# Optimization experiments

Hardware: AMD Instinct MI355X
Metric: run time of the kernel (lower is better)

The kernel has to match this reference:

```python
import jax, jax.numpy as jnp
import numpy as np

B, T, D, H = 4, 2048, 512, 8
DK = D // H

def setup_inputs() -> dict:
    key = jax.random.key(0)
    ks = jax.random.split(key, 5)
    s = 1.0 / np.sqrt(D)
    return {
        "x": jax.random.normal(ks[0], (B, T, D), dtype=jnp.float32),
        "Wq": jax.random.normal(ks[1], (D, D), dtype=jnp.float32) * s,
        "bq": jnp.zeros((D,), dtype=jnp.float32),
        "Wk": jax.random.normal(ks[2], (D, D), dtype=jnp.float32) * s,
        "bk": jnp.zeros((D,), dtype=jnp.float32),
        "Wv": jax.random.normal(ks[3], (D, D), dtype=jnp.float32) * s,
        "bv": jnp.zeros((D,), dtype=jnp.float32),
        "Wo": jax.random.normal(ks[4], (D, D), dtype=jnp.float32) * s,
        "bo": jnp.zeros((D,), dtype=jnp.float32),
    }

def reference(x, Wq, bq, Wk, bk, Wv, bv, Wo, bo):
    # Linear projections (torch Linear: x @ W.T + b); split into heads.
    q = (x @ Wq.T + bq).reshape(B, T, H, DK)  # [B,T,H,dk]
    k = (x @ Wk.T + bk).reshape(B, T, H, DK)
    v = (x @ Wv.T + bv).reshape(B, T, H, DK)
    scale = 1.0 / np.sqrt(DK)
    # scores: [B,H,T,T]
    scores = jnp.einsum("bqhd,bkhd->bhqk", q, k) * scale
    attn = jax.nn.softmax(scores, axis=-1)
    ctx = jnp.einsum("bhqk,bkhd->bqhd", attn, v).reshape(B, T, D)
    return ctx @ Wo.T + bo
```

## Files before the change

kernel.cpp:

```cpp
#include <hip/hip_runtime.h>
#include <stdint.h>

#define NB 4
#define NT 2048
#define ND 512
#define NH 8
#define NDK 64
#define NM (NB*NT)

typedef __attribute__((ext_vector_type(8))) short short8;
typedef __attribute__((ext_vector_type(4))) float f32x4;

__device__ __forceinline__ unsigned short f2b(float f) {
    union { float f; uint32_t u; } v; v.f = f;
    return (unsigned short)((v.u + 0x7FFFu + ((v.u >> 16) & 1u)) >> 16);
}

__device__ __forceinline__ void load_lds16(const void* g, void* l) {
    void* gn = const_cast<void*>(g);
    __builtin_amdgcn_global_load_lds((__attribute__((address_space(1))) void*)gn,
                                     (__attribute__((address_space(3))) void*)l,
                                     16, 0, 0);
}

__global__ void convert_all(const float* __restrict__ x,  const float* __restrict__ wq,
                            const float* __restrict__ wk, const float* __restrict__ wv,
                            const float* __restrict__ wo, unsigned short* __restrict__ dst) {
    size_t i = ((size_t)blockIdx.x * 256 + threadIdx.x) * 4;
    const float* src; size_t off;
    if (i < 4194304) { src = x; off = i; }
    else {
        size_t j = i - 4194304;
        src = (j < 262144) ? wq : (j < 524288) ? wk : (j < 786432) ? wv : wo;
        off = j & 262143;
    }
    f32x4 v = *(const f32x4*)(src + off);
    ushort4 r;
    r.x = f2b(v[0]); r.y = f2b(v[1]); r.z = f2b(v[2]); r.w = f2b(v[3]);
    *(ushort4*)(dst + i) = r;
}

__global__ __launch_bounds__(256, 3) void proj_gemm(
        const unsigned short* __restrict__ X,
        const unsigned short* __restrict__ Wbase,
        const float* __restrict__ bias0, const float* __restrict__ bias1,
        const float* __restrict__ bias2,
        unsigned short* __restrict__ Obase, unsigned short* __restrict__ VTb,
        float scale0) {
    const int z = blockIdx.z;
    const float* bias = (z == 0) ? bias0 : (z == 1 ? bias1 : bias2);
    const float scale = (z == 0) ? scale0 : 1.0f;

    int rowBase, colBase;
    const unsigned short *Ap, *Bp;
    if (z == 2) {
        rowBase = blockIdx.x * 128;  colBase = blockIdx.y * 128;
        Ap = Wbase + 2 * (ND * ND);  Bp = X;
    } else {
        rowBase = blockIdx.y * 128;  colBase = blockIdx.x * 128;
        Ap = X;                      Bp = Wbase + (size_t)z * (ND * ND);
    }

    __shared__ alignas(16) unsigned short ldsA[128 * 64];
    __shared__ alignas(16) unsigned short ldsW[128 * 64];

    const int tid = threadIdx.x;
    const int lane = tid & 63, wave = tid >> 6;
    const int quad = lane >> 4, l15 = lane & 15;
    const int wm = wave >> 1, wn = wave & 1;

    const int rS = tid >> 3;
    const int gc = (tid & 7) ^ (rS & 7);
    const unsigned short* gA = Ap + (size_t)(rowBase + rS) * ND + gc * 8;
    const unsigned short* gW = Bp + (size_t)(colBase + rS) * ND + gc * 8;
    const int ldst = wave * 512;

    const int swz = l15 & 7;

    f32x4 acc[4][4];
#pragma unroll
    for (int i = 0; i < 4; i++)
#pragma unroll
        for (int j = 0; j < 4; j++) acc[i][j] = (f32x4)0.0f;

    for (int kt = 0; kt < ND / 64; ++kt) {
        __syncthreads();
#pragma unroll
        for (int c = 0; c < 4; ++c) {
            load_lds16(gA + (size_t)c * 32 * ND, ldsA + c * 2048 + ldst);
            load_lds16(gW + (size_t)c * 32 * ND, ldsW + c * 2048 + ldst);
        }
        gA += 64; gW += 64;
        __syncthreads();

#pragma unroll
        for (int ks = 0; ks < 2; ++ks) {
            short8 af[4], bfm[4];
#pragma unroll
            for (int mt = 0; mt < 4; ++mt)
                af[mt] = *(const short8*)(ldsA + (wm * 64 + mt * 16 + l15) * 64
                                          + (((ks * 4 + quad) ^ swz) * 8));
#pragma unroll
            for (int nt = 0; nt < 4; ++nt)
                bfm[nt] = *(const short8*)(ldsW + (wn * 64 + nt * 16 + l15) * 64
                                           + (((ks * 4 + quad) ^ swz) * 8));
#pragma unroll
            for (int mt = 0; mt < 4; ++mt)
#pragma unroll
                for (int nt = 0; nt < 4; ++nt)
                    acc[mt][nt] = __builtin_amdgcn_mfma_f32_16x16x32_bf16(
                        af[mt], bfm[nt], acc[mt][nt], 0, 0, 0);
        }
    }

    if (z == 2) {
        const int bz = colBase >> 11;
        const int t0 = colBase & 2047;
        unsigned short* VTo = VTb + ((size_t)(bz * 512 + rowBase)) * NT + t0;
#pragma unroll
        for (int mt = 0; mt < 4; mt++)
#pragma unroll
            for (int reg = 0; reg < 4; reg++) {
                int m = wm * 64 + mt * 16 + quad * 4 + reg;
                float bm = bias[rowBase + m];
                unsigned short* dst = VTo + (size_t)m * NT + wn * 64 + l15;
#pragma unroll
                for (int nt = 0; nt < 4; nt++)
                    dst[nt * 16] = f2b(acc[mt][nt][reg] + bm);
            }
    } else {
        float biasr[4];
#pragma unroll
        for (int nt = 0; nt < 4; nt++)
            biasr[nt] = bias[colBase + wn * 64 + nt * 16 + l15];
        unsigned short* Oz = Obase + (size_t)z * ((size_t)NM * ND);
#pragma unroll
        for (int mt = 0; mt < 4; mt++) {
            int row = rowBase + wm * 64 + mt * 16 + quad * 4;
#pragma unroll
            for (int reg = 0; reg < 4; reg++) {
                unsigned short* dst = Oz + (size_t)(row + reg) * ND + colBase + wn * 64 + l15;
#pragma unroll
                for (int nt = 0; nt < 4; nt++)
                    dst[nt * 16] = f2b((acc[mt][nt][reg] + biasr[nt]) * scale);
            }
        }
    }
}

__global__ __launch_bounds__(256, 4) void out_gemm(
        const unsigned short* __restrict__ A, const unsigned short* __restrict__ W,
        const float* __restrict__ bias, float* __restrict__ OF) {
    __shared__ alignas(16) unsigned short ldsA[64 * 64];
    __shared__ alignas(16) unsigned short ldsW[128 * 64];

    const int tid = threadIdx.x;
    const int lane = tid & 63, wave = tid >> 6;
    const int quad = lane >> 4, l15 = lane & 15;
    const int wm = wave >> 1, wn = wave & 1;
    const int rowBase = blockIdx.y * 64;
    const int colBase = blockIdx.x * 128;

    const int rS = tid >> 3;
    const int gc = (tid & 7) ^ (rS & 7);
    const unsigned short* gA = A + (size_t)(rowBase + rS) * ND + gc * 8;
    const unsigned short* gW = W + (size_t)(colBase + rS) * ND + gc * 8;
    const int ldst = wave * 512;
    const int swz = l15 & 7;

    f32x4 acc[2][4];
#pragma unroll
    for (int mt = 0; mt < 2; mt++)
#pragma unroll
        for (int nt = 0; nt < 4; nt++) acc[mt][nt] = (f32x4)0.0f;

    for (int kt = 0; kt < ND / 64; ++kt) {
        __syncthreads();
#pragma unroll
        for (int c = 0; c < 2; ++c)
            load_lds16(gA + (size_t)c * 32 * ND, ldsA + c * 2048 + ldst);
#pragma unroll
        for (int c = 0; c < 4; ++c)
            load_lds16(gW + (size_t)c * 32 * ND, ldsW + c * 2048 + ldst);
        gA += 64; gW += 64;
        __syncthreads();

#pragma unroll
        for (int ks = 0; ks < 2; ++ks) {
            short8 af[2], bfm[4];
#pragma unroll
            for (int mt = 0; mt < 2; ++mt)
                af[mt] = *(const short8*)(ldsA + (wm * 32 + mt * 16 + l15) * 64
                                          + (((ks * 4 + quad) ^ swz) * 8));
#pragma unroll
            for (int nt = 0; nt < 4; ++nt)
                bfm[nt] = *(const short8*)(ldsW + (wn * 64 + nt * 16 + l15) * 64
                                           + (((ks * 4 + quad) ^ swz) * 8));
#pragma unroll
            for (int mt = 0; mt < 2; ++mt)
#pragma unroll
                for (int nt = 0; nt < 4; ++nt)
                    acc[mt][nt] = __builtin_amdgcn_mfma_f32_16x16x32_bf16(
                        af[mt], bfm[nt], acc[mt][nt], 0, 0, 0);
        }
    }

    float biasr[4];
#pragma unroll
    for (int nt = 0; nt < 4; nt++)
        biasr[nt] = bias[colBase + wn * 64 + nt * 16 + l15];

#pragma unroll
    for (int mt = 0; mt < 2; mt++)
#pragma unroll
        for (int reg = 0; reg < 4; reg++) {
            int row = rowBase + wm * 32 + mt * 16 + quad * 4 + reg;
            float* dst = OF + (size_t)row * ND + colBase + wn * 64 + l15;
#pragma unroll
            for (int nt = 0; nt < 4; nt++)
                dst[nt * 16] = acc[mt][nt][reg] + biasr[nt];
        }
}

__global__ __launch_bounds__(512, 4) void attn_kernel(
        const unsigned short* __restrict__ Qb, const unsigned short* __restrict__ Kb,
        const unsigned short* __restrict__ VTb, unsigned short* __restrict__ Cb) {
    const int L = blockIdx.x + 16 * (blockIdx.y + 8 * blockIdx.z);
    const int s = L >> 3;
    const int qt = s & 15;
    const int g = (L & 7) + 8 * (s >> 4);
    const int h = g & 7, b = g >> 3;

    __shared__ alignas(16) unsigned short Ks[2 * 8192];
    __shared__ alignas(16) unsigned short Vt[2 * 8192];

    const int tid = threadIdx.x, lane = tid & 63, wave = tid >> 6;
    const int wq = wave & 3, half = wave >> 2;
    const int quad = lane >> 4, l15 = lane & 15;
    const size_t headOff = (size_t)h * NDK;
    const size_t rowB = (size_t)b * NT;
    const unsigned short* VT = VTb + (size_t)(b * NH + h) * ((size_t)NDK * NT);

    short8 aq[2][2];
#pragma unroll
    for (int t = 0; t < 2; ++t)
#pragma unroll
        for (int ks = 0; ks < 2; ++ks)
            aq[t][ks] = *(const short8*)(Qb
                + (rowB + qt * 128 + wq * 32 + t * 16 + l15) * ND
                + headOff + ks * 32 + quad * 8);

    const int rK = tid >> 3;
    const int rb = rK & 31;
    const int kap = (rb < 16) ? ((rb >> 2) * 8 + (rb & 3))
                              : (((rb - 16) >> 2) * 8 + 4 + ((rb - 16) & 3));
    const int gK8 = (tid & 7) ^ (rK & 7);
    const unsigned short* gK = Kb + (rowB + (rK & 32) + kap) * ND + headOff + gK8 * 8;
    const int rV = tid >> 4;
    const int gV8 = (tid & 15) ^ (rV & 7);
    const unsigned short* gV = VT + (size_t)rV * NT + gV8 * 8;
    const int ldst = wave * 512;

    const int swz = l15 & 7;
    const int ko0 = l15 * 64 + ((quad ^ swz) * 8);
    const int ko1 = l15 * 64 + (((4 + quad) ^ swz) * 8);

    f32x4 o[2][4];
#pragma unroll
    for (int t = 0; t < 2; ++t)
#pragma unroll
        for (int nt = 0; nt < 4; ++nt) o[t][nt] = (f32x4)0.0f;
    float lacc[2] = {0.0f, 0.0f};

    auto STAGE = [&](int bb, int r) {
        const unsigned short* k = gK + (size_t)r * 128 * ND;
        const unsigned short* v = gV + (size_t)r * 128;
        unsigned short* kd = Ks + bb * 8192 + ldst;
        unsigned short* vd = Vt + bb * 8192 + ldst;
#pragma unroll
        for (int c = 0; c < 2; ++c) {
            load_lds16(k + (size_t)c * 64 * ND, kd + c * 4096);
            load_lds16(v + (size_t)c * 32 * NT, vd + c * 4096);
        }
    };

    STAGE(0, 0);
    __syncthreads();

    for (int kv = 0; kv < 16; ++kv) {
        const int buf = kv & 1;
        if (kv < 15) STAGE(buf ^ 1, kv + 1);

        const unsigned short* KB = Ks + buf * 8192;
        const unsigned short* VB = Vt + buf * 8192;
        __builtin_amdgcn_s_setprio(1);
#pragma unroll
        for (int pp = 0; pp < 2; ++pp) {
            const int pb = half * 2 + pp;
            short8 kA0 = *(const short8*)(KB + pb * 2048 + ko0);
            short8 kA1 = *(const short8*)(KB + pb * 2048 + ko1);
            short8 kB0 = *(const short8*)(KB + pb * 2048 + 1024 + ko0);
            short8 kB1 = *(const short8*)(KB + pb * 2048 + 1024 + ko1);
            const int vo = l15 * 128 + (((pb * 4 + quad) ^ swz) * 8);
            short8 vf[4];
#pragma unroll
            for (int nt = 0; nt < 4; ++nt)
                vf[nt] = *(const short8*)(VB + vo + nt * 2048);

#pragma unroll
            for (int t = 0; t < 2; ++t) {
                f32x4 sa = (f32x4)0.0f, sb = (f32x4)0.0f;
                sa = __builtin_amdgcn_mfma_f32_16x16x32_bf16(kA0, aq[t][0], sa, 0, 0, 0);
                sa = __builtin_amdgcn_mfma_f32_16x16x32_bf16(kA1, aq[t][1], sa, 0, 0, 0);
                sb = __builtin_amdgcn_mfma_f32_16x16x32_bf16(kB0, aq[t][0], sb, 0, 0, 0);
                sb = __builtin_amdgcn_mfma_f32_16x16x32_bf16(kB1, aq[t][1], sb, 0, 0, 0);
                float pA0 = __builtin_amdgcn_exp2f(sa[0]), pA1 = __builtin_amdgcn_exp2f(sa[1]);
                float pA2 = __builtin_amdgcn_exp2f(sa[2]), pA3 = __builtin_amdgcn_exp2f(sa[3]);
                float pB0 = __builtin_amdgcn_exp2f(sb[0]), pB1 = __builtin_amdgcn_exp2f(sb[1]);
                float pB2 = __builtin_amdgcn_exp2f(sb[2]), pB3 = __builtin_amdgcn_exp2f(sb[3]);
                lacc[t] += ((pA0 + pA1) + (pA2 + pA3)) + ((pB0 + pB1) + (pB2 + pB3));
                union { uint32_t w[4]; short8 v; } cv;
                cv.w[0] = __builtin_amdgcn_perm(__float_as_uint(pA1), __float_as_uint(pA0), 0x07060302u);
                cv.w[1] = __builtin_amdgcn_perm(__float_as_uint(pA3), __float_as_uint(pA2), 0x07060302u);
                cv.w[2] = __builtin_amdgcn_perm(__float_as_uint(pB1), __float_as_uint(pB0), 0x07060302u);
                cv.w[3] = __builtin_amdgcn_perm(__float_as_uint(pB3), __float_as_uint(pB2), 0x07060302u);
#pragma unroll
                for (int nt = 0; nt < 4; ++nt)
                    o[t][nt] = __builtin_amdgcn_mfma_f32_16x16x32_bf16(
                        cv.v, vf[nt], o[t][nt], 0, 0, 0);
            }
        }
        __builtin_amdgcn_s_setprio(0);
        __syncthreads();
    }

    f32x4* sc4 = (f32x4*)Ks;
    float* scl = (float*)Vt;
    const int lx = lane & 7;
    if (half) {
#pragma unroll
        for (int t = 0; t < 2; ++t) {
            scl[(wq * 64 + lane) * 2 + t] = lacc[t];
#pragma unroll
            for (int nt = 0; nt < 4; ++nt)
                sc4[(wq * 64 + lane) * 8 + ((t * 4 + nt) ^ lx)] = o[t][nt];
        }
    }
    __syncthreads();
    if (!half) {
#pragma unroll
        for (int t = 0; t < 2; ++t) {
            float la = lacc[t] + scl[(wq * 64 + lane) * 2 + t];
            la += __shfl_xor(la, 16);
            la += __shfl_xor(la, 32);
#pragma unroll
            for (int nt = 0; nt < 4; ++nt)
                o[t][nt] += sc4[(wq * 64 + lane) * 8 + ((t * 4 + nt) ^ lx)];
#pragma unroll
            for (int reg = 0; reg < 4; ++reg) {
                float inv = 1.0f / __shfl(la, quad * 4 + reg);
                size_t row = rowB + qt * 128 + wq * 32 + t * 16 + quad * 4 + reg;
#pragma unroll
                for (int nt = 0; nt < 4; ++nt)
                    Cb[row * ND + headOff + nt * 16 + l15] = f2b(o[t][nt][reg] * inv);
            }
        }
    }
}

extern "C" void kernel_launch(void* const* d_in, const int* in_sizes, int n_in,
                              void* d_out, int out_size, void* d_ws, size_t ws_size,
                              hipStream_t stream) {
    (void)in_sizes; (void)n_in; (void)out_size; (void)ws_size;
    const float* x  = (const float*)d_in[0];
    const float* Wq = (const float*)d_in[1];
    const float* bq = (const float*)d_in[2];
    const float* Wk = (const float*)d_in[3];
    const float* bk = (const float*)d_in[4];
    const float* Wv = (const float*)d_in[5];
    const float* bv = (const float*)d_in[6];
    const float* Wo = (const float*)d_in[7];
    const float* bo = (const float*)d_in[8];
    float* out = (float*)d_out;

    unsigned short* ws  = (unsigned short*)d_ws;
    unsigned short* xb  = ws;
    unsigned short* wqb = xb + 4194304;
    unsigned short* Qb  = wqb + 4 * 262144;
    unsigned short* Kb  = Qb + 4194304;
    unsigned short* VTb = Kb + 4194304;
    unsigned short* Cb  = VTb + 4194304;
    unsigned short* wob = wqb + 3 * 262144;

    convert_all<<<5120, 256, 0, stream>>>(x, Wq, Wk, Wv, Wo, ws);

    const float qscale = 0.125f * 1.44269504f;
    proj_gemm<<<dim3(4, 64, 3), 256, 0, stream>>>(xb, wqb, bq, bk, bv, Qb, VTb, qscale);
    attn_kernel<<<dim3(16, 8, 4), 512, 0, stream>>>(Qb, Kb, VTb, Cb);
    out_gemm<<<dim3(4, 128), 256, 0, stream>>>(Cb, wob, bo, out);
}
```

Baseline: 149.9 us.

## Double attention query tile per block and compute row sums with MFMA

Each attention block now handles 256 query rows instead of 128, so every K/V tile staged in LDS is reused by twice as many queries and the grid halves. The softmax denominator is now accumulated with an extra MFMA against a vector of bf16 ones, replacing the scalar exp-sum and cross-lane shuffles. The cross-half output reduction is split into two LDS rounds to fit the larger accumulator set. Register pressure roughly doubles (launch bounds lowered to 2 blocks per CU), which reduces occupancy and leaves 256 blocks for the GPU.

```diff
diff --git a/kernel.cpp b/kernel.cpp
--- a/kernel.cpp
+++ b/kernel.cpp
@@ -222,13 +222,13 @@
         }
 }
 
-__global__ __launch_bounds__(512, 4) void attn_kernel(
+__global__ __launch_bounds__(512, 2) void attn_kernel(
         const unsigned short* __restrict__ Qb, const unsigned short* __restrict__ Kb,
         const unsigned short* __restrict__ VTb, unsigned short* __restrict__ Cb) {
-    const int L = blockIdx.x + 16 * (blockIdx.y + 8 * blockIdx.z);
+    const int L = blockIdx.x + 8 * (blockIdx.y + 8 * blockIdx.z);
     const int s = L >> 3;
-    const int qt = s & 15;
-    const int g = (L & 7) + 8 * (s >> 4);
+    const int qt = s & 7;
+    const int g = (L & 7) + 8 * (s >> 3);
     const int h = g & 7, b = g >> 3;
 
     __shared__ alignas(16) unsigned short Ks[2 * 8192];
@@ -241,13 +241,13 @@
     const size_t rowB = (size_t)b * NT;
     const unsigned short* VT = VTb + (size_t)(b * NH + h) * ((size_t)NDK * NT);
 
-    short8 aq[2][2];
-#pragma unroll
-    for (int t = 0; t < 2; ++t)
+    short8 aq[4][2];
+#pragma unroll
+    for (int t = 0; t < 4; ++t)
 #pragma unroll
         for (int ks = 0; ks < 2; ++ks)
             aq[t][ks] = *(const short8*)(Qb
-                + (rowB + qt * 128 + wq * 32 + t * 16 + l15) * ND
+                + (rowB + qt * 256 + wq * 64 + t * 16 + l15) * ND
                 + headOff + ks * 32 + quad * 8);
 
     const int rK = tid >> 3;
@@ -265,12 +265,17 @@
     const int ko0 = l15 * 64 + ((quad ^ swz) * 8);
     const int ko1 = l15 * 64 + (((4 + quad) ^ swz) * 8);
 
-    f32x4 o[2][4];
-#pragma unroll
-    for (int t = 0; t < 2; ++t)
+    const short8 ones = {0x3F80, 0x3F80, 0x3F80, 0x3F80,
+                         0x3F80, 0x3F80, 0x3F80, 0x3F80};
+
+    f32x4 o[4][4];
+#pragma unroll
+    for (int t = 0; t < 4; ++t)
 #pragma unroll
         for (int nt = 0; nt < 4; ++nt) o[t][nt] = (f32x4)0.0f;
-    float lacc[2] = {0.0f, 0.0f};
+    f32x4 lsum[4];
+#pragma unroll
+    for (int t = 0; t < 4; ++t) lsum[t] = (f32x4)0.0f;
 
     auto STAGE = [&](int bb, int r) {
         const unsigned short* k = gK + (size_t)r * 128 * ND;
@@ -308,7 +313,7 @@
                 vf[nt] = *(const short8*)(VB + vo + nt * 2048);
 
 #pragma unroll
-            for (int t = 0; t < 2; ++t) {
+            for (int t = 0; t < 4; ++t) {
                 f32x4 sa = (f32x4)0.0f, sb = (f32x4)0.0f;
                 sa = __builtin_amdgcn_mfma_f32_16x16x32_bf16(kA0, aq[t][0], sa, 0, 0, 0);
                 sa = __builtin_amdgcn_mfma_f32_16x16x32_bf16(kA1, aq[t][1], sa, 0, 0, 0);
@@ -318,12 +323,13 @@
                 float pA2 = __builtin_amdgcn_exp2f(sa[2]), pA3 = __builtin_amdgcn_exp2f(sa[3]);
                 float pB0 = __builtin_amdgcn_exp2f(sb[0]), pB1 = __builtin_amdgcn_exp2f(sb[1]);
                 float pB2 = __builtin_amdgcn_exp2f(sb[2]), pB3 = __builtin_amdgcn_exp2f(sb[3]);
-                lacc[t] += ((pA0 + pA1) + (pA2 + pA3)) + ((pB0 + pB1) + (pB2 + pB3));
                 union { uint32_t w[4]; short8 v; } cv;
                 cv.w[0] = __builtin_amdgcn_perm(__float_as_uint(pA1), __float_as_uint(pA0), 0x07060302u);
                 cv.w[1] = __builtin_amdgcn_perm(__float_as_uint(pA3), __float_as_uint(pA2), 0x07060302u);
                 cv.w[2] = __builtin_amdgcn_perm(__float_as_uint(pB1), __float_as_uint(pB0), 0x07060302u);
                 cv.w[3] = __builtin_amdgcn_perm(__float_as_uint(pB3), __float_as_uint(pB2), 0x07060302u);
+                lsum[t] = __builtin_amdgcn_mfma_f32_16x16x32_bf16(
+                    cv.v, ones, lsum[t], 0, 0, 0);
 #pragma unroll
                 for (int nt = 0; nt < 4; ++nt)
                     o[t][nt] = __builtin_amdgcn_mfma_f32_16x16x32_bf16(
@@ -334,37 +340,58 @@
         __syncthreads();
     }
 
-    f32x4* sc4 = (f32x4*)Ks;
-    float* scl = (float*)Vt;
+    f32x4* sc4  = (f32x4*)Ks;
+    f32x4* scl4 = (f32x4*)Vt;
     const int lx = lane & 7;
+    const int base = wq * 64 + lane;
+
     if (half) {
 #pragma unroll
-        for (int t = 0; t < 2; ++t) {
-            scl[(wq * 64 + lane) * 2 + t] = lacc[t];
-#pragma unroll
-            for (int nt = 0; nt < 4; ++nt)
-                sc4[(wq * 64 + lane) * 8 + ((t * 4 + nt) ^ lx)] = o[t][nt];
-        }
+        for (int t = 0; t < 4; ++t)
+            scl4[base * 4 + (t ^ (lane & 3))] = lsum[t];
+#pragma unroll
+        for (int t = 0; t < 2; ++t)
+#pragma unroll
+            for (int nt = 0; nt < 4; ++nt)
+                sc4[base * 8 + ((t * 4 + nt) ^ lx)] = o[t][nt];
     }
     __syncthreads();
     if (!half) {
 #pragma unroll
-        for (int t = 0; t < 2; ++t) {
-            float la = lacc[t] + scl[(wq * 64 + lane) * 2 + t];
-            la += __shfl_xor(la, 16);
-            la += __shfl_xor(la, 32);
-#pragma unroll
-            for (int nt = 0; nt < 4; ++nt)
-                o[t][nt] += sc4[(wq * 64 + lane) * 8 + ((t * 4 + nt) ^ lx)];
+        for (int t = 0; t < 4; ++t)
+            lsum[t] += scl4[base * 4 + (t ^ (lane & 3))];
+#pragma unroll
+        for (int t = 0; t < 2; ++t)
+#pragma unroll
+            for (int nt = 0; nt < 4; ++nt)
+                o[t][nt] += sc4[base * 8 + ((t * 4 + nt) ^ lx)];
+    }
+    __syncthreads();
+    if (half) {
+#pragma unroll
+        for (int t = 2; t < 4; ++t)
+#pragma unroll
+            for (int nt = 0; nt < 4; ++nt)
+                sc4[base * 8 + (((t - 2) * 4 + nt) ^ lx)] = o[t][nt];
+    }
+    __syncthreads();
+    if (!half) {
+#pragma unroll
+        for (int t = 2; t < 4; ++t)
+#pragma unroll
+            for (int nt = 0; nt < 4; ++nt)
+                o[t][nt] += sc4[base * 8 + (((t - 2) * 4 + nt) ^ lx)];
+
+#pragma unroll
+        for (int t = 0; t < 4; ++t)
 #pragma unroll
             for (int reg = 0; reg < 4; ++reg) {
-                float inv = 1.0f / __shfl(la, quad * 4 + reg);
-                size_t row = rowB + qt * 128 + wq * 32 + t * 16 + quad * 4 + reg;
+                float inv = 1.0f / lsum[t][reg];
+                size_t row = rowB + qt * 256 + wq * 64 + t * 16 + quad * 4 + reg;
 #pragma unroll
                 for (int nt = 0; nt < 4; ++nt)
                     Cb[row * ND + headOff + nt * 16 + l15] = f2b(o[t][nt][reg] * inv);
             }
-        }
     }
 }
 
@@ -396,6 +423,6 @@
 
     const float qscale = 0.125f * 1.44269504f;
     proj_gemm<<<dim3(4, 64, 3), 256, 0, stream>>>(xb, wqb, bq, bk, bv, Qb, VTb, qscale);
-    attn_kernel<<<dim3(16, 8, 4), 512, 0, stream>>>(Qb, Kb, VTb, Cb);
+    attn_kernel<<<dim3(8, 8, 4), 512, 0, stream>>>(Qb, Kb, VTb, Cb);
     out_gemm<<<dim3(4, 128), 256, 0, stream>>>(Cb, wob, bo, out);
 }
```

Measured after the change: 150.9 us. Within noise of the previous version (+0.7%).
